# Performance work log

Hardware: AMD Instinct MI355X
Metric: run time of the kernel (lower is better)

## Reference

```python
import jax, jax.numpy as jnp
import numpy as np

B, L, D, M, S = 1024, 50, 64, 100000, 2
NEG = float(-2**32 + 1)

def _ln(x):
    # F.layer_norm over last dim, no affine, eps=1e-8 (biased variance)
    mu = x.mean(-1, keepdims=True)
    var = ((x - mu) ** 2).mean(-1, keepdims=True)
    return (x - mu) / jnp.sqrt(var + 1e-8)

def setup_inputs():
    key = jax.random.key(0)
    ks = jax.random.split(key, 24)
    p = lambda i, shape: jax.random.normal(ks[i], shape, jnp.float32) * 0.05
    return {
        'user_items': jax.random.randint(ks[0], (B, L), 0, M + 1),
        'pos_items': jax.random.randint(ks[1], (B, L), 0, M + 1),
        'neg_items': jax.random.randint(ks[2], (B, L), 0, M + 1),
        'padding_mask': jnp.ones((B, L, 1), jnp.float32),
        'item_embedding': p(3, (M + 1, D)),
        'pos_embedding': p(4, (L, D)),
        'Q_sabs': p(5, (S, D, D)),
        'K_sabs': p(6, (S, D, D)),
        'V_sabs': p(7, (S, D, D)),
        'c1_w': p(8, (S, L, L)), 'c1_b': p(9, (S, L)),
        'c2_w': p(10, (S, L, L)), 'c2_b': p(11, (S, L)),
        'query_item': p(12, (1, 1, D)),
        'K_lba': p(13, (D, D)), 'V_lba': p(14, (D, D)),
        'l1_w': p(15, (1, 1)), 'l1_b': p(16, (1,)),
        'l2_w': p(17, (1, 1)), 'l2_b': p(18, (1,)),
        'gated_weight': p(19, (3 * D, 1)),
        'gated_bias': p(20, (1, 1)),
    }

def _forward(user_items, pos_items, neg_items, padding_mask, item_embedding,
             pos_embedding, Q_sabs, K_sabs, V_sabs, c1_w, c1_b, c2_w, c2_b,
             query_item, K_lba, V_lba, l1_w, l1_b, l2_w, l2_b,
             gated_weight, gated_bias):
    ie = item_embedding[user_items]                      # [B,L,D]
    inputs = ie + pos_embedding[None]                    # add positional (dropout = identity)
    inputs = inputs * padding_mask
    inputs = _ln(inputs)

    tril = jnp.tril(jnp.ones((L, L), inputs.dtype))
    key_mask = jnp.transpose(padding_mask, (0, 2, 1))    # [B,1,L]
    scale = D ** 0.5

    x = inputs
    for i in range(S):
        Qx = x @ Q_sabs[i]; Kx = x @ K_sabs[i]; Vx = x @ V_sabs[i]
        scores = jnp.einsum('bqd,bkd->bqk', Qx, Kx) / scale      # [B,L,L]
        scores = jnp.where(tril[None] == 0, NEG, scores)          # causal mask
        scores = jnp.where(key_mask == 0, NEG, scores)            # key padding mask
        scores = scores * padding_mask                            # query mask (NO softmax, as in source)
        att = jnp.einsum('bqk,bkd->bqd', scores, Vx) + x          # residual
        att = _ln(att)
        # Conv1d(L, L, 1) mixes across the sequence-position axis
        h = jax.nn.relu(jnp.einsum('ij,bjd->bid', c1_w[i], att) + c1_b[i][None, :, None])
        ff = jnp.einsum('ij,bjd->bid', c2_w[i], h) + c2_b[i][None, :, None] + att
        ff = ff * padding_mask
        x = _ln(ff)
    loc = x                                                       # [B,L,D]

    # location-based attention: single learned query over sequence
    Kx = inputs @ K_lba; Vx = inputs @ V_lba
    sc = jnp.einsum('qd,bld->bql', query_item[0], Kx)             # [B,1,L]
    sc = jnp.where(key_mask == 0, NEG, sc)
    sc = jax.nn.softmax(sc, axis=-1)
    glo = jnp.einsum('bql,bld->bqd', sc, Vx)                      # [B,1,D]
    glo = _ln(glo)
    h = jax.nn.relu(l1_w[0, 0] * glo + l1_b[0])                   # Conv1d(1,1,1) = scalar affine
    glo = l2_w[0, 0] * h + l2_b[0] + glo
    glo = _ln(glo)

    pos_e = item_embedding[pos_items]                             # [B,L,D]
    neg_e = item_embedding[neg_items]
    ms = jnp.concatenate([ie, ie], 0)                             # tile [2,1,1]
    y = jnp.tile(glo, (2, L, 1))                                  # [2B,L,D]
    mi = jnp.concatenate([pos_e, neg_e], 0)
    cat = jnp.concatenate([ms, y, mi], -1).reshape(-1, 3 * D)
    logits = (cat @ gated_weight + gated_bias).reshape(2 * B, L, 1)
    gating = jax.nn.sigmoid(jax.nn.sigmoid(logits))               # double sigmoid, as in source

    tl = jnp.concatenate([loc, loc], 0)
    tg = jnp.tile(glo, (2, 1, 1))
    out = tl * gating + tg * (1.0 - gating)
    out = out * jnp.concatenate([padding_mask, padding_mask], 0)
    out = _ln(out)
    op, on = out[:B], out[B:]
    return jnp.stack([jnp.sum(op * pos_e, -1), jnp.sum(on * neg_e, -1)], 0)  # [2,B,L]

def reference(user_items, pos_items, neg_items, padding_mask, item_embedding,
              pos_embedding, Q_sabs, K_sabs, V_sabs, c1_w, c1_b, c2_w, c2_b,
              query_item, K_lba, V_lba, l1_w, l1_b, l2_w, l2_b,
              gated_weight, gated_bias):
    return _forward(user_items, pos_items, neg_items, padding_mask, item_embedding,
                    pos_embedding, Q_sabs, K_sabs, V_sabs, c1_w, c1_b, c2_w, c2_b,
                    query_item, K_lba, V_lba, l1_w, l1_b, l2_w, l2_b,
                    gated_weight, gated_bias)
```

## Files before the change

kernel.cpp:

```cpp
#include <hip/hip_runtime.h>


#define NB 1024
#define LL 50
#define DD 64
#define LD 66
#define LDC 52
#define NR 7
#define NEGV (-4294967295.0f)

__device__ __forceinline__ float wsum(float v) {
#pragma unroll
  for (int m = 32; m >= 1; m >>= 1) v += __shfl_xor(v, m, 64);
  return v;
}
__device__ __forceinline__ float wmax(float v) {
#pragma unroll
  for (int m = 32; m >= 1; m >>= 1) v = fmaxf(v, __shfl_xor(v, m, 64));
  return v;
}
__device__ __forceinline__ float rowln(float v) {
  float m = wsum(v) * (1.f / 64.f);
  float df = v - m;
  float var = wsum(df * df) * (1.f / 64.f);
  return df / sqrtf(var + 1e-8f);
}
__device__ __forceinline__ float2 ld2(const float* p) {
  return *reinterpret_cast<const float2*>(p);
}

__global__ __launch_bounds__(512, 6) void fissa_kernel(
    const int* __restrict__ user_items, const int* __restrict__ pos_items,
    const int* __restrict__ neg_items, const float* __restrict__ pmask,
    const float* __restrict__ item_emb, const float* __restrict__ pos_emb,
    const float* __restrict__ Qs, const float* __restrict__ Ks,
    const float* __restrict__ Vs, const float* __restrict__ c1w,
    const float* __restrict__ c1b, const float* __restrict__ c2w,
    const float* __restrict__ c2b, const float* __restrict__ query,
    const float* __restrict__ Klba, const float* __restrict__ Vlba,
    const float* __restrict__ l1w, const float* __restrict__ l1b,
    const float* __restrict__ l2w, const float* __restrict__ l2b,
    const float* __restrict__ gw, const float* __restrict__ gb,
    float* __restrict__ out) {
  __shared__ float s_x[LL * LD];
  __shared__ float s_a[LL * LD];
  __shared__ float s_b[LL * LD];
  __shared__ float s_c[LL * LDC];
  __shared__ float s_mask[64], s_bias[64], s_qv[64], s_glo[64], s_gw[192], s_scal[2];

  const int b = blockIdx.x;
  const int tid = threadIdx.x;
  const int wv = tid >> 6, ln = tid & 63;

  int qrow[NR], qoff[NR], coff[NR];
  bool qok[NR];
#pragma unroll
  for (int r = 0; r < NR; ++r) {
    int q = wv + 8 * r;
    qok[r] = (q < LL);
    qrow[r] = qok[r] ? q : (LL - 1);
    qoff[r] = qrow[r] * LD;
    coff[r] = qrow[r] * LDC;
  }

  if (tid < 64) s_mask[tid] = (tid < LL) ? pmask[b * LL + tid] : 0.f;
  else if (tid < 128) s_qv[tid - 64] = query[tid - 64];
  else if (tid < 320) s_gw[tid - 128] = gw[tid - 128];

#pragma unroll
  for (int r = 0; r < NR; ++r) {
    int l = qrow[r];
    int u = user_items[b * LL + l];
    float mk = pmask[b * LL + l];
    float v = (item_emb[(size_t)u * DD + ln] + pos_emb[l * DD + ln]) * mk;
    float o = rowln(v);
    if (qok[r]) s_x[qoff[r] + ln] = o;
  }
  __syncthreads();

  {
    float akl[NR], avl[NR];
#pragma unroll
    for (int r = 0; r < NR; ++r) { akl[r] = 0.f; avl[r] = 0.f; }
    const float* Kc = Klba + ln;
    const float* Vc = Vlba + ln;
#pragma unroll 2
    for (int k = 0; k < DD; k += 2) {
      float wk0 = Kc[k * DD], wk1 = Kc[(k + 1) * DD];
      float wv0 = Vc[k * DD], wv1 = Vc[(k + 1) * DD];
#pragma unroll
      for (int r = 0; r < NR; ++r) {
        float2 xv = ld2(&s_x[qoff[r] + k]);
        akl[r] = fmaf(xv.x, wk0, akl[r]);
        akl[r] = fmaf(xv.y, wk1, akl[r]);
        avl[r] = fmaf(xv.x, wv0, avl[r]);
        avl[r] = fmaf(xv.y, wv1, avl[r]);
      }
    }
#pragma unroll
    for (int r = 0; r < NR; ++r)
      if (qok[r]) { s_a[qoff[r] + ln] = akl[r]; s_b[qoff[r] + ln] = avl[r]; }
  }
  __syncthreads();
  if (wv == 0) {
    float sc = -INFINITY;
    if (ln < LL) {
      float acc = 0.f;
      const float* arow = &s_a[ln * LD];
#pragma unroll
      for (int d = 0; d < DD; d += 2) {
        float2 av = ld2(&arow[d]);
        acc = fmaf(s_qv[d], av.x, acc);
        acc = fmaf(s_qv[d + 1], av.y, acc);
      }
      sc = acc;
      if (s_mask[ln] == 0.f) sc = NEGV;
    }
    float mx = wmax(sc);
    float e = (ln < LL) ? expf(sc - mx) : 0.f;
    float den = wsum(e);
    if (ln < LL) s_bias[ln] = e / den;
    float acc = 0.f;
#pragma unroll 2
    for (int l = 0; l < LL; ++l) acc = fmaf(s_bias[l], s_b[l * LD + ln], acc);
    float g = rowln(acc);
    float h = fmaxf(l1w[0] * g + l1b[0], 0.f);
    float glo = rowln(l2w[0] * h + l2b[0] + g);
    s_glo[ln] = glo;
    float gs = wsum(glo * s_gw[64 + ln]);
    if (ln == 0) s_scal[0] = gs + gb[0];
  }
  __syncthreads();

  for (int i = 0; i < 2; ++i) {
    const float* Qc = Qs + i * DD * DD + ln;
    const float* Kc = Ks + i * DD * DD + ln;
    const float* Vc = Vs + i * DD * DD + ln;

    {
      float aq[NR], ak[NR];
#pragma unroll
      for (int r = 0; r < NR; ++r) { aq[r] = 0.f; ak[r] = 0.f; }
#pragma unroll 2
      for (int k = 0; k < DD; k += 2) {
        float wq0 = Qc[k * DD], wq1 = Qc[(k + 1) * DD];
        float wk0 = Kc[k * DD], wk1 = Kc[(k + 1) * DD];
#pragma unroll
        for (int r = 0; r < NR; ++r) {
          float2 xv = ld2(&s_x[qoff[r] + k]);
          aq[r] = fmaf(xv.x, wq0, aq[r]);
          aq[r] = fmaf(xv.y, wq1, aq[r]);
          ak[r] = fmaf(xv.x, wk0, ak[r]);
          ak[r] = fmaf(xv.y, wk1, ak[r]);
        }
      }
#pragma unroll
      for (int r = 0; r < NR; ++r)
        if (qok[r]) { s_a[qoff[r] + ln] = aq[r]; s_b[qoff[r] + ln] = ak[r]; }
    }
    __syncthreads();

    {
      float sc[NR];
#pragma unroll
      for (int r = 0; r < NR; ++r) sc[r] = 0.f;
      const int kk = (ln < LL) ? ln : (LL - 1);
      const float* krow = &s_b[kk * LD];
#pragma unroll 2
      for (int d = 0; d < DD; d += 2) {
        float2 kv = ld2(&krow[d]);
#pragma unroll
        for (int r = 0; r < NR; ++r) {
          float2 qv = ld2(&s_a[qoff[r] + d]);
          sc[r] = fmaf(qv.x, kv.x, sc[r]);
          sc[r] = fmaf(qv.y, kv.y, sc[r]);
        }
      }
      if (ln < LL) {
        float mk = s_mask[ln];
#pragma unroll
        for (int r = 0; r < NR; ++r)
          if (qok[r]) {
            float v = sc[r] * 0.125f;
            if (ln > qrow[r]) v = NEGV;
            if (mk == 0.f) v = NEGV;
            v *= s_mask[qrow[r]];
            s_c[coff[r] + ln] = v;
          }
      }
    }
    __syncthreads();

    {
      float av[NR];
#pragma unroll
      for (int r = 0; r < NR; ++r) av[r] = 0.f;
#pragma unroll 2
      for (int k = 0; k < DD; k += 2) {
        float wv0 = Vc[k * DD], wv1 = Vc[(k + 1) * DD];
#pragma unroll
        for (int r = 0; r < NR; ++r) {
          float2 xv = ld2(&s_x[qoff[r] + k]);
          av[r] = fmaf(xv.x, wv0, av[r]);
          av[r] = fmaf(xv.y, wv1, av[r]);
        }
      }
#pragma unroll
      for (int r = 0; r < NR; ++r)
        if (qok[r]) s_a[qoff[r] + ln] = av[r];
    }
    __syncthreads();

    {
      float at[NR];
#pragma unroll
      for (int r = 0; r < NR; ++r) at[r] = s_x[qoff[r] + ln];
#pragma unroll 2
      for (int k = 0; k < LL; k += 2) {
        float v0 = s_a[k * LD + ln];
        float v1 = s_a[(k + 1) * LD + ln];
#pragma unroll
        for (int r = 0; r < NR; ++r) {
          float2 sv = ld2(&s_c[coff[r] + k]);
          at[r] = fmaf(sv.x, v0, at[r]);
          at[r] = fmaf(sv.y, v1, at[r]);
        }
      }
#pragma unroll
      for (int r = 0; r < NR; ++r) {
        float o = rowln(at[r]);
        if (qok[r]) s_x[qoff[r] + ln] = o;
      }
    }
    __syncthreads();

    for (int e = tid; e < LL * LL; e += 512) {
      int q = e / LL;
      s_c[q * LDC + (e - q * LL)] = c1w[i * LL * LL + e];
    }
    if (tid < LL) s_bias[tid] = c1b[i * LL + tid];
    __syncthreads();

    {
      float hh[NR];
#pragma unroll
      for (int r = 0; r < NR; ++r) hh[r] = 0.f;
#pragma unroll 2
      for (int j = 0; j < LL; j += 2) {
        float x0 = s_x[j * LD + ln];
        float x1 = s_x[(j + 1) * LD + ln];
#pragma unroll
        for (int r = 0; r < NR; ++r) {
          float2 cv = ld2(&s_c[coff[r] + j]);
          hh[r] = fmaf(cv.x, x0, hh[r]);
          hh[r] = fmaf(cv.y, x1, hh[r]);
        }
      }
#pragma unroll
      for (int r = 0; r < NR; ++r)
        if (qok[r]) s_b[qoff[r] + ln] = fmaxf(hh[r] + s_bias[qrow[r]], 0.f);
    }
    __syncthreads();

    for (int e = tid; e < LL * LL; e += 512) {
      int q = e / LL;
      s_c[q * LDC + (e - q * LL)] = c2w[i * LL * LL + e];
    }
    if (tid < LL) s_bias[tid] = c2b[i * LL + tid];
    __syncthreads();

    {
      float f0[NR];
#pragma unroll
      for (int r = 0; r < NR; ++r) f0[r] = s_x[qoff[r] + ln];
#pragma unroll 2
      for (int j = 0; j < LL; j += 2) {
        float h0 = s_b[j * LD + ln];
        float h1 = s_b[(j + 1) * LD + ln];
#pragma unroll
        for (int r = 0; r < NR; ++r) {
          float2 cv = ld2(&s_c[coff[r] + j]);
          f0[r] = fmaf(cv.x, h0, f0[r]);
          f0[r] = fmaf(cv.y, h1, f0[r]);
        }
      }
#pragma unroll
      for (int r = 0; r < NR; ++r) {
        float v = (f0[r] + s_bias[qrow[r]]) * s_mask[qrow[r]];
        float o = rowln(v);
        if (qok[r]) s_x[qoff[r] + ln] = o;
      }
    }
    __syncthreads();
  }

  float g2c = s_scal[0];
  float gloc = s_glo[ln];
  for (int row = wv; row < 2 * LL; row += 8) {
    int sgn = row >= LL;
    int l = row - sgn * LL;
    int u = user_items[b * LL + l];
    int it = sgn ? neg_items[b * LL + l] : pos_items[b * LL + l];
    float ie_d = item_emb[(size_t)u * DD + ln];
    float mi_d = item_emb[(size_t)it * DD + ln];
    float logit = wsum(ie_d * s_gw[ln] + mi_d * s_gw[128 + ln]) + g2c;
    float sg = 1.f / (1.f + expf(-logit));
    float g = 1.f / (1.f + expf(-sg));
    float od = (s_x[l * LD + ln] * g + gloc * (1.f - g)) * s_mask[l];
    float o = rowln(od);
    float res = wsum(o * mi_d);
    if (ln == 0) out[(sgn * NB + b) * LL + l] = res;
  }
}

extern "C" void kernel_launch(void* const* d_in, const int* in_sizes, int n_in,
                              void* d_out, int out_size, void* d_ws, size_t ws_size,
                              hipStream_t stream) {
  const int* user_items = (const int*)d_in[0];
  const int* pos_items = (const int*)d_in[1];
  const int* neg_items = (const int*)d_in[2];
  const float* pmask = (const float*)d_in[3];
  const float* item_emb = (const float*)d_in[4];
  const float* pos_emb = (const float*)d_in[5];
  const float* Qs = (const float*)d_in[6];
  const float* Ks = (const float*)d_in[7];
  const float* Vs = (const float*)d_in[8];
  const float* c1w = (const float*)d_in[9];
  const float* c1b = (const float*)d_in[10];
  const float* c2w = (const float*)d_in[11];
  const float* c2b = (const float*)d_in[12];
  const float* query = (const float*)d_in[13];
  const float* Klba = (const float*)d_in[14];
  const float* Vlba = (const float*)d_in[15];
  const float* l1w = (const float*)d_in[16];
  const float* l1b = (const float*)d_in[17];
  const float* l2w = (const float*)d_in[18];
  const float* l2b = (const float*)d_in[19];
  const float* gw = (const float*)d_in[20];
  const float* gb = (const float*)d_in[21];
  float* out = (float*)d_out;

  fissa_kernel<<<dim3(NB), dim3(512), 0, stream>>>(
      user_items, pos_items, neg_items, pmask, item_emb, pos_emb, Qs, Ks, Vs,
      c1w, c1b, c2w, c2b, query, Klba, Vlba, l1w, l1b, l2w, l2b, gw, gb, out);
}
```

Measured before the change: 408.4 us.

## Read conv weights via wave-uniform scalar loads instead of staging in LDS

The c1/c2 weight matrices are no longer copied into shared memory with extra barriers. Each wave now reads its rows directly from global memory using wave-uniform row indices (readfirstlane), so the loads can go through the scalar path. The change also fully unrolls the inner loops, widens the attention-times-V loop to float4 shared-memory loads, and lowers the launch-bounds occupancy hint from 6 to 4 waves to allow more registers. This removes two barrier-separated copy phases per layer, at the cost of more register pressure and reliance on scalar cache hits.

```diff
diff --git a/kernel.cpp b/kernel.cpp
--- a/kernel.cpp
+++ b/kernel.cpp
@@ -28,8 +28,11 @@
 __device__ __forceinline__ float2 ld2(const float* p) {
   return *reinterpret_cast<const float2*>(p);
 }
-
-__global__ __launch_bounds__(512, 6) void fissa_kernel(
+__device__ __forceinline__ float4 ld4(const float* p) {
+  return *reinterpret_cast<const float4*>(p);
+}
+
+__global__ __launch_bounds__(512, 4) void fissa_kernel(
     const int* __restrict__ user_items, const int* __restrict__ pos_items,
     const int* __restrict__ neg_items, const float* __restrict__ pmask,
     const float* __restrict__ item_emb, const float* __restrict__ pos_emb,
@@ -46,13 +49,13 @@
   __shared__ float s_a[LL * LD];
   __shared__ float s_b[LL * LD];
   __shared__ float s_c[LL * LDC];
-  __shared__ float s_mask[64], s_bias[64], s_qv[64], s_glo[64], s_gw[192], s_scal[2];
+  __shared__ float s_mask[64], s_qv[64], s_glo[64], s_gw[192], s_sm[64], s_scal[2];
 
   const int b = blockIdx.x;
   const int tid = threadIdx.x;
   const int wv = tid >> 6, ln = tid & 63;
 
-  int qrow[NR], qoff[NR], coff[NR];
+  int qrow[NR], qoff[NR], coff[NR], qu[NR];
   bool qok[NR];
 #pragma unroll
   for (int r = 0; r < NR; ++r) {
@@ -61,6 +64,7 @@
     qrow[r] = qok[r] ? q : (LL - 1);
     qoff[r] = qrow[r] * LD;
     coff[r] = qrow[r] * LDC;
+    qu[r] = __builtin_amdgcn_readfirstlane(qrow[r]);
   }
 
   if (tid < 64) s_mask[tid] = (tid < LL) ? pmask[b * LL + tid] : 0.f;
@@ -84,7 +88,7 @@
     for (int r = 0; r < NR; ++r) { akl[r] = 0.f; avl[r] = 0.f; }
     const float* Kc = Klba + ln;
     const float* Vc = Vlba + ln;
-#pragma unroll 2
+#pragma unroll
     for (int k = 0; k < DD; k += 2) {
       float wk0 = Kc[k * DD], wk1 = Kc[(k + 1) * DD];
       float wv0 = Vc[k * DD], wv1 = Vc[(k + 1) * DD];
@@ -119,10 +123,10 @@
     float mx = wmax(sc);
     float e = (ln < LL) ? expf(sc - mx) : 0.f;
     float den = wsum(e);
-    if (ln < LL) s_bias[ln] = e / den;
+    if (ln < LL) s_sm[ln] = e / den;
     float acc = 0.f;
-#pragma unroll 2
-    for (int l = 0; l < LL; ++l) acc = fmaf(s_bias[l], s_b[l * LD + ln], acc);
+#pragma unroll
+    for (int l = 0; l < LL; ++l) acc = fmaf(s_sm[l], s_b[l * LD + ln], acc);
     float g = rowln(acc);
     float h = fmaxf(l1w[0] * g + l1b[0], 0.f);
     float glo = rowln(l2w[0] * h + l2b[0] + g);
@@ -132,6 +136,7 @@
   }
   __syncthreads();
 
+#pragma unroll 1
   for (int i = 0; i < 2; ++i) {
     const float* Qc = Qs + i * DD * DD + ln;
     const float* Kc = Ks + i * DD * DD + ln;
@@ -141,7 +146,7 @@
       float aq[NR], ak[NR];
 #pragma unroll
       for (int r = 0; r < NR; ++r) { aq[r] = 0.f; ak[r] = 0.f; }
-#pragma unroll 2
+#pragma unroll
       for (int k = 0; k < DD; k += 2) {
         float wq0 = Qc[k * DD], wq1 = Qc[(k + 1) * DD];
         float wk0 = Kc[k * DD], wk1 = Kc[(k + 1) * DD];
@@ -166,7 +171,7 @@
       for (int r = 0; r < NR; ++r) sc[r] = 0.f;
       const int kk = (ln < LL) ? ln : (LL - 1);
       const float* krow = &s_b[kk * LD];
-#pragma unroll 2
+#pragma unroll
       for (int d = 0; d < DD; d += 2) {
         float2 kv = ld2(&krow[d]);
 #pragma unroll
@@ -195,7 +200,7 @@
       float av[NR];
 #pragma unroll
       for (int r = 0; r < NR; ++r) av[r] = 0.f;
-#pragma unroll 2
+#pragma unroll
       for (int k = 0; k < DD; k += 2) {
         float wv0 = Vc[k * DD], wv1 = Vc[(k + 1) * DD];
 #pragma unroll
@@ -215,15 +220,29 @@
       float at[NR];
 #pragma unroll
       for (int r = 0; r < NR; ++r) at[r] = s_x[qoff[r] + ln];
-#pragma unroll 2
-      for (int k = 0; k < LL; k += 2) {
+#pragma unroll
+      for (int k = 0; k < 48; k += 4) {
         float v0 = s_a[k * LD + ln];
         float v1 = s_a[(k + 1) * LD + ln];
-#pragma unroll
-        for (int r = 0; r < NR; ++r) {
-          float2 sv = ld2(&s_c[coff[r] + k]);
+        float v2 = s_a[(k + 2) * LD + ln];
+        float v3 = s_a[(k + 3) * LD + ln];
+#pragma unroll
+        for (int r = 0; r < NR; ++r) {
+          float4 sv = ld4(&s_c[coff[r] + k]);
           at[r] = fmaf(sv.x, v0, at[r]);
           at[r] = fmaf(sv.y, v1, at[r]);
+          at[r] = fmaf(sv.z, v2, at[r]);
+          at[r] = fmaf(sv.w, v3, at[r]);
+        }
+      }
+      {
+        float v0 = s_a[48 * LD + ln];
+        float v1 = s_a[49 * LD + ln];
+#pragma unroll
+        for (int r = 0; r < NR; ++r) {
+          float2 sv = ld2(&s_c[coff[r] + 48]);
+          at[r] = fmaf(sv.x, v0, at[r]);
+          at[r] = fmaf(sv.y, v1, at[r]);
         }
       }
 #pragma unroll
@@ -234,59 +253,43 @@
     }
     __syncthreads();
 
-    for (int e = tid; e < LL * LL; e += 512) {
-      int q = e / LL;
-      s_c[q * LDC + (e - q * LL)] = c1w[i * LL * LL + e];
-    }
-    if (tid < LL) s_bias[tid] = c1b[i * LL + tid];
-    __syncthreads();
-
-    {
+    {
+      const float* c1r[NR];
       float hh[NR];
 #pragma unroll
-      for (int r = 0; r < NR; ++r) hh[r] = 0.f;
-#pragma unroll 2
-      for (int j = 0; j < LL; j += 2) {
-        float x0 = s_x[j * LD + ln];
-        float x1 = s_x[(j + 1) * LD + ln];
-#pragma unroll
-        for (int r = 0; r < NR; ++r) {
-          float2 cv = ld2(&s_c[coff[r] + j]);
-          hh[r] = fmaf(cv.x, x0, hh[r]);
-          hh[r] = fmaf(cv.y, x1, hh[r]);
-        }
+      for (int r = 0; r < NR; ++r) {
+        c1r[r] = c1w + i * LL * LL + qu[r] * LL;
+        hh[r] = 0.f;
+      }
+#pragma unroll
+      for (int j = 0; j < LL; ++j) {
+        float xj = s_x[j * LD + ln];
+#pragma unroll
+        for (int r = 0; r < NR; ++r) hh[r] = fmaf(c1r[r][j], xj, hh[r]);
       }
 #pragma unroll
       for (int r = 0; r < NR; ++r)
-        if (qok[r]) s_b[qoff[r] + ln] = fmaxf(hh[r] + s_bias[qrow[r]], 0.f);
-    }
-    __syncthreads();
-
-    for (int e = tid; e < LL * LL; e += 512) {
-      int q = e / LL;
-      s_c[q * LDC + (e - q * LL)] = c2w[i * LL * LL + e];
-    }
-    if (tid < LL) s_bias[tid] = c2b[i * LL + tid];
-    __syncthreads();
-
-    {
+        if (qok[r]) s_b[qoff[r] + ln] = fmaxf(hh[r] + c1b[i * LL + qu[r]], 0.f);
+    }
+    __syncthreads();
+
+    {
+      const float* c2r[NR];
       float f0[NR];
 #pragma unroll
-      for (int r = 0; r < NR; ++r) f0[r] = s_x[qoff[r] + ln];
-#pragma unroll 2
-      for (int j = 0; j < LL; j += 2) {
-        float h0 = s_b[j * LD + ln];
-        float h1 = s_b[(j + 1) * LD + ln];
-#pragma unroll
-        for (int r = 0; r < NR; ++r) {
-          float2 cv = ld2(&s_c[coff[r] + j]);
-          f0[r] = fmaf(cv.x, h0, f0[r]);
-          f0[r] = fmaf(cv.y, h1, f0[r]);
-        }
-      }
-#pragma unroll
-      for (int r = 0; r < NR; ++r) {
-        float v = (f0[r] + s_bias[qrow[r]]) * s_mask[qrow[r]];
+      for (int r = 0; r < NR; ++r) {
+        c2r[r] = c2w + i * LL * LL + qu[r] * LL;
+        f0[r] = s_x[qoff[r] + ln];
+      }
+#pragma unroll
+      for (int j = 0; j < LL; ++j) {
+        float hj = s_b[j * LD + ln];
+#pragma unroll
+        for (int r = 0; r < NR; ++r) f0[r] = fmaf(c2r[r][j], hj, f0[r]);
+      }
+#pragma unroll
+      for (int r = 0; r < NR; ++r) {
+        float v = (f0[r] + c2b[i * LL + qu[r]]) * s_mask[qrow[r]];
         float o = rowln(v);
         if (qok[r]) s_x[qoff[r] + ln] = o;
       }
@@ -296,6 +299,7 @@
 
   float g2c = s_scal[0];
   float gloc = s_glo[ln];
+#pragma unroll 1
   for (int row = wv; row < 2 * LL; row += 8) {
     int sgn = row >= LL;
     int l = row - sgn * LL;
```

Result: slower. 1.124 ms (+175.2%).

## Store K transposed in LDS, vectorize inner loops with float4, relax launch bounds

Applied to the files above, without the earlier changes.

Pads activation rows to 68 floats so float4 LDS loads are aligned, and widens all inner GEMM-like loops to process four k-steps per iteration with float4 reads. K projections are written transposed into a new s_kt buffer so score computation reads keys with unit stride per lane, and the s_a buffer is removed by reusing s_b. Launch bounds drop from 6 to 2 blocks per SM, which gives the compiler more registers but may lower occupancy. The nested fma chains also change the summation order slightly.

```diff
diff --git a/kernel.cpp b/kernel.cpp
--- a/kernel.cpp
+++ b/kernel.cpp
@@ -4,7 +4,8 @@
 #define NB 1024
 #define LL 50
 #define DD 64
-#define LD 66
+#define LD 68
+#define LDT 51
 #define LDC 52
 #define NR 7
 #define NEGV (-4294967295.0f)
@@ -28,8 +29,11 @@
 __device__ __forceinline__ float2 ld2(const float* p) {
   return *reinterpret_cast<const float2*>(p);
 }
-
-__global__ __launch_bounds__(512, 6) void fissa_kernel(
+__device__ __forceinline__ float4 ld4(const float* p) {
+  return *reinterpret_cast<const float4*>(p);
+}
+
+__global__ __launch_bounds__(512, 2) void fissa_kernel(
     const int* __restrict__ user_items, const int* __restrict__ pos_items,
     const int* __restrict__ neg_items, const float* __restrict__ pmask,
     const float* __restrict__ item_emb, const float* __restrict__ pos_emb,
@@ -42,11 +46,12 @@
     const float* __restrict__ l2w, const float* __restrict__ l2b,
     const float* __restrict__ gw, const float* __restrict__ gb,
     float* __restrict__ out) {
-  __shared__ float s_x[LL * LD];
-  __shared__ float s_a[LL * LD];
-  __shared__ float s_b[LL * LD];
-  __shared__ float s_c[LL * LDC];
-  __shared__ float s_mask[64], s_bias[64], s_qv[64], s_glo[64], s_gw[192], s_scal[2];
+  __shared__ __align__(16) float s_x[LL * LD];
+  __shared__ __align__(16) float s_b[LL * LD];
+  __shared__ __align__(16) float s_kt[DD * LDT + 64];
+  __shared__ __align__(16) float s_c[LL * LDC];
+  __shared__ __align__(16) float s_mask[64], s_qv[64], s_glo[64], s_sm[64],
+      s_bias[64], s_gw[192], s_scal[2];
 
   const int b = blockIdx.x;
   const int tid = threadIdx.x;
@@ -85,44 +90,43 @@
     const float* Kc = Klba + ln;
     const float* Vc = Vlba + ln;
 #pragma unroll 2
-    for (int k = 0; k < DD; k += 2) {
-      float wk0 = Kc[k * DD], wk1 = Kc[(k + 1) * DD];
-      float wv0 = Vc[k * DD], wv1 = Vc[(k + 1) * DD];
+    for (int kc = 0; kc < DD; kc += 4) {
+      float wk0 = Kc[kc * DD], wk1 = Kc[(kc + 1) * DD];
+      float wk2 = Kc[(kc + 2) * DD], wk3 = Kc[(kc + 3) * DD];
+      float wv0 = Vc[kc * DD], wv1 = Vc[(kc + 1) * DD];
+      float wv2 = Vc[(kc + 2) * DD], wv3 = Vc[(kc + 3) * DD];
 #pragma unroll
       for (int r = 0; r < NR; ++r) {
-        float2 xv = ld2(&s_x[qoff[r] + k]);
-        akl[r] = fmaf(xv.x, wk0, akl[r]);
-        akl[r] = fmaf(xv.y, wk1, akl[r]);
-        avl[r] = fmaf(xv.x, wv0, avl[r]);
-        avl[r] = fmaf(xv.y, wv1, avl[r]);
+        float4 xv = ld4(&s_x[qoff[r] + kc]);
+        akl[r] = fmaf(xv.x, wk0, fmaf(xv.y, wk1, fmaf(xv.z, wk2, fmaf(xv.w, wk3, akl[r]))));
+        avl[r] = fmaf(xv.x, wv0, fmaf(xv.y, wv1, fmaf(xv.z, wv2, fmaf(xv.w, wv3, avl[r]))));
       }
     }
 #pragma unroll
     for (int r = 0; r < NR; ++r)
-      if (qok[r]) { s_a[qoff[r] + ln] = akl[r]; s_b[qoff[r] + ln] = avl[r]; }
+      if (qok[r]) {
+        s_kt[ln * LDT + qrow[r]] = akl[r];
+        s_b[qoff[r] + ln] = avl[r];
+      }
   }
   __syncthreads();
+
   if (wv == 0) {
     float sc = -INFINITY;
-    if (ln < LL) {
+    {
       float acc = 0.f;
-      const float* arow = &s_a[ln * LD];
-#pragma unroll
-      for (int d = 0; d < DD; d += 2) {
-        float2 av = ld2(&arow[d]);
-        acc = fmaf(s_qv[d], av.x, acc);
-        acc = fmaf(s_qv[d + 1], av.y, acc);
-      }
+#pragma unroll 4
+      for (int d = 0; d < DD; ++d) acc = fmaf(s_qv[d], s_kt[d * LDT + ln], acc);
       sc = acc;
-      if (s_mask[ln] == 0.f) sc = NEGV;
+      if (ln >= LL || s_mask[ln] == 0.f) sc = (ln < LL) ? NEGV : -INFINITY;
     }
     float mx = wmax(sc);
     float e = (ln < LL) ? expf(sc - mx) : 0.f;
     float den = wsum(e);
-    if (ln < LL) s_bias[ln] = e / den;
+    if (ln < LL) s_sm[ln] = e / den;
     float acc = 0.f;
 #pragma unroll 2
-    for (int l = 0; l < LL; ++l) acc = fmaf(s_bias[l], s_b[l * LD + ln], acc);
+    for (int l = 0; l < LL; ++l) acc = fmaf(s_sm[l], s_b[l * LD + ln], acc);
     float g = rowln(acc);
     float h = fmaxf(l1w[0] * g + l1b[0], 0.f);
     float glo = rowln(l2w[0] * h + l2b[0] + g);
@@ -132,6 +136,7 @@
   }
   __syncthreads();
 
+#pragma unroll 1
   for (int i = 0; i < 2; ++i) {
     const float* Qc = Qs + i * DD * DD + ln;
     const float* Kc = Ks + i * DD * DD + ln;
@@ -142,21 +147,24 @@
 #pragma unroll
       for (int r = 0; r < NR; ++r) { aq[r] = 0.f; ak[r] = 0.f; }
 #pragma unroll 2
-      for (int k = 0; k < DD; k += 2) {
-        float wq0 = Qc[k * DD], wq1 = Qc[(k + 1) * DD];
-        float wk0 = Kc[k * DD], wk1 = Kc[(k + 1) * DD];
-#pragma unroll
-        for (int r = 0; r < NR; ++r) {
-          float2 xv = ld2(&s_x[qoff[r] + k]);
-          aq[r] = fmaf(xv.x, wq0, aq[r]);
-          aq[r] = fmaf(xv.y, wq1, aq[r]);
-          ak[r] = fmaf(xv.x, wk0, ak[r]);
-          ak[r] = fmaf(xv.y, wk1, ak[r]);
+      for (int kc = 0; kc < DD; kc += 4) {
+        float wq0 = Qc[kc * DD], wq1 = Qc[(kc + 1) * DD];
+        float wq2 = Qc[(kc + 2) * DD], wq3 = Qc[(kc + 3) * DD];
+        float wk0 = Kc[kc * DD], wk1 = Kc[(kc + 1) * DD];
+        float wk2 = Kc[(kc + 2) * DD], wk3 = Kc[(kc + 3) * DD];
+#pragma unroll
+        for (int r = 0; r < NR; ++r) {
+          float4 xv = ld4(&s_x[qoff[r] + kc]);
+          aq[r] = fmaf(xv.x, wq0, fmaf(xv.y, wq1, fmaf(xv.z, wq2, fmaf(xv.w, wq3, aq[r]))));
+          ak[r] = fmaf(xv.x, wk0, fmaf(xv.y, wk1, fmaf(xv.z, wk2, fmaf(xv.w, wk3, ak[r]))));
         }
       }
 #pragma unroll
       for (int r = 0; r < NR; ++r)
-        if (qok[r]) { s_a[qoff[r] + ln] = aq[r]; s_b[qoff[r] + ln] = ak[r]; }
+        if (qok[r]) {
+          s_b[qoff[r] + ln] = aq[r];
+          s_kt[ln * LDT + qrow[r]] = ak[r];
+        }
     }
     __syncthreads();
 
@@ -164,16 +172,16 @@
       float sc[NR];
 #pragma unroll
       for (int r = 0; r < NR; ++r) sc[r] = 0.f;
-      const int kk = (ln < LL) ? ln : (LL - 1);
-      const float* krow = &s_b[kk * LD];
-#pragma unroll 2
-      for (int d = 0; d < DD; d += 2) {
-        float2 kv = ld2(&krow[d]);
-#pragma unroll
-        for (int r = 0; r < NR; ++r) {
-          float2 qv = ld2(&s_a[qoff[r] + d]);
-          sc[r] = fmaf(qv.x, kv.x, sc[r]);
-          sc[r] = fmaf(qv.y, kv.y, sc[r]);
+#pragma unroll 2
+      for (int dc = 0; dc < DD; dc += 4) {
+        float k0 = s_kt[dc * LDT + ln];
+        float k1 = s_kt[(dc + 1) * LDT + ln];
+        float k2 = s_kt[(dc + 2) * LDT + ln];
+        float k3 = s_kt[(dc + 3) * LDT + ln];
+#pragma unroll
+        for (int r = 0; r < NR; ++r) {
+          float4 qv = ld4(&s_b[qoff[r] + dc]);
+          sc[r] = fmaf(qv.x, k0, fmaf(qv.y, k1, fmaf(qv.z, k2, fmaf(qv.w, k3, sc[r]))));
         }
       }
       if (ln < LL) {
@@ -196,18 +204,18 @@
 #pragma unroll
       for (int r = 0; r < NR; ++r) av[r] = 0.f;
 #pragma unroll 2
-      for (int k = 0; k < DD; k += 2) {
-        float wv0 = Vc[k * DD], wv1 = Vc[(k + 1) * DD];
-#pragma unroll
-        for (int r = 0; r < NR; ++r) {
-          float2 xv = ld2(&s_x[qoff[r] + k]);
-          av[r] = fmaf(xv.x, wv0, av[r]);
-          av[r] = fmaf(xv.y, wv1, av[r]);
+      for (int kc = 0; kc < DD; kc += 4) {
+        float wv0 = Vc[kc * DD], wv1 = Vc[(kc + 1) * DD];
+        float wv2 = Vc[(kc + 2) * DD], wv3 = Vc[(kc + 3) * DD];
+#pragma unroll
+        for (int r = 0; r < NR; ++r) {
+          float4 xv = ld4(&s_x[qoff[r] + kc]);
+          av[r] = fmaf(xv.x, wv0, fmaf(xv.y, wv1, fmaf(xv.z, wv2, fmaf(xv.w, wv3, av[r]))));
         }
       }
 #pragma unroll
       for (int r = 0; r < NR; ++r)
-        if (qok[r]) s_a[qoff[r] + ln] = av[r];
+        if (qok[r]) s_b[qoff[r] + ln] = av[r];
     }
     __syncthreads();
 
@@ -216,14 +224,24 @@
 #pragma unroll
       for (int r = 0; r < NR; ++r) at[r] = s_x[qoff[r] + ln];
 #pragma unroll 2
-      for (int k = 0; k < LL; k += 2) {
-        float v0 = s_a[k * LD + ln];
-        float v1 = s_a[(k + 1) * LD + ln];
-#pragma unroll
-        for (int r = 0; r < NR; ++r) {
-          float2 sv = ld2(&s_c[coff[r] + k]);
-          at[r] = fmaf(sv.x, v0, at[r]);
-          at[r] = fmaf(sv.y, v1, at[r]);
+      for (int k = 0; k < 48; k += 4) {
+        float v0 = s_b[k * LD + ln];
+        float v1 = s_b[(k + 1) * LD + ln];
+        float v2 = s_b[(k + 2) * LD + ln];
+        float v3 = s_b[(k + 3) * LD + ln];
+#pragma unroll
+        for (int r = 0; r < NR; ++r) {
+          float4 sv = ld4(&s_c[coff[r] + k]);
+          at[r] = fmaf(sv.x, v0, fmaf(sv.y, v1, fmaf(sv.z, v2, fmaf(sv.w, v3, at[r]))));
+        }
+      }
+      {
+        float v0 = s_b[48 * LD + ln];
+        float v1 = s_b[49 * LD + ln];
+#pragma unroll
+        for (int r = 0; r < NR; ++r) {
+          float2 sv = ld2(&s_c[coff[r] + 48]);
+          at[r] = fmaf(sv.x, v0, fmaf(sv.y, v1, at[r]));
         }
       }
 #pragma unroll
@@ -246,14 +264,24 @@
 #pragma unroll
       for (int r = 0; r < NR; ++r) hh[r] = 0.f;
 #pragma unroll 2
-      for (int j = 0; j < LL; j += 2) {
+      for (int j = 0; j < 48; j += 4) {
         float x0 = s_x[j * LD + ln];
         float x1 = s_x[(j + 1) * LD + ln];
-#pragma unroll
-        for (int r = 0; r < NR; ++r) {
-          float2 cv = ld2(&s_c[coff[r] + j]);
-          hh[r] = fmaf(cv.x, x0, hh[r]);
-          hh[r] = fmaf(cv.y, x1, hh[r]);
+        float x2 = s_x[(j + 2) * LD + ln];
+        float x3 = s_x[(j + 3) * LD + ln];
+#pragma unroll
+        for (int r = 0; r < NR; ++r) {
+          float4 cv = ld4(&s_c[coff[r] + j]);
+          hh[r] = fmaf(cv.x, x0, fmaf(cv.y, x1, fmaf(cv.z, x2, fmaf(cv.w, x3, hh[r]))));
+        }
+      }
+      {
+        float x0 = s_x[48 * LD + ln];
+        float x1 = s_x[49 * LD + ln];
+#pragma unroll
+        for (int r = 0; r < NR; ++r) {
+          float2 cv = ld2(&s_c[coff[r] + 48]);
+          hh[r] = fmaf(cv.x, x0, fmaf(cv.y, x1, hh[r]));
         }
       }
 #pragma unroll
@@ -274,14 +302,24 @@
 #pragma unroll
       for (int r = 0; r < NR; ++r) f0[r] = s_x[qoff[r] + ln];
 #pragma unroll 2
-      for (int j = 0; j < LL; j += 2) {
+      for (int j = 0; j < 48; j += 4) {
         float h0 = s_b[j * LD + ln];
         float h1 = s_b[(j + 1) * LD + ln];
-#pragma unroll
-        for (int r = 0; r < NR; ++r) {
-          float2 cv = ld2(&s_c[coff[r] + j]);
-          f0[r] = fmaf(cv.x, h0, f0[r]);
-          f0[r] = fmaf(cv.y, h1, f0[r]);
+        float h2 = s_b[(j + 2) * LD + ln];
+        float h3 = s_b[(j + 3) * LD + ln];
+#pragma unroll
+        for (int r = 0; r < NR; ++r) {
+          float4 cv = ld4(&s_c[coff[r] + j]);
+          f0[r] = fmaf(cv.x, h0, fmaf(cv.y, h1, fmaf(cv.z, h2, fmaf(cv.w, h3, f0[r]))));
+        }
+      }
+      {
+        float h0 = s_b[48 * LD + ln];
+        float h1 = s_b[49 * LD + ln];
+#pragma unroll
+        for (int r = 0; r < NR; ++r) {
+          float2 cv = ld2(&s_c[coff[r] + 48]);
+          f0[r] = fmaf(cv.x, h0, fmaf(cv.y, h1, f0[r]));
         }
       }
 #pragma unroll
@@ -296,6 +334,7 @@
 
   float g2c = s_scal[0];
   float gloc = s_glo[ln];
+#pragma unroll 1
   for (int row = wv; row < 2 * LL; row += 8) {
     int sgn = row >= LL;
     int l = row - sgn * LL;
```

New measurement: 342.9 us. -16.0%, faster.
